# Kernel tuning notes

Hardware: AMD Instinct MI355X
Metric: run time of the kernel (lower is better)

## Reference

```python
import jax, jax.numpy as jnp
import numpy as np

N, E, D, R, H = 50000, 200000, 128, 4, 64

def setup_inputs() -> dict:
    key = jax.random.key(0)
    ks = jax.random.split(key, 12)
    s = 0.02
    return {
        'node_feature': jax.random.normal(ks[0], (N, D), dtype=jnp.float32),
        'edge_src': jax.random.randint(ks[1], (E,), 0, N, dtype=jnp.int32),
        'edge_dst': jax.random.randint(ks[2], (E,), 0, N, dtype=jnp.int32),
        'edge_type': jax.random.randint(ks[3], (E,), 0, R, dtype=jnp.int32),
        'Wr1': s * jax.random.normal(ks[4], (R, D, H), dtype=jnp.float32),
        'br1': jnp.zeros((R, H), dtype=jnp.float32),
        'Wr2': s * jax.random.normal(ks[5], (R, H, H), dtype=jnp.float32),
        'br2': jnp.zeros((R, H), dtype=jnp.float32),
        'Wr3': s * jax.random.normal(ks[6], (R, H, D), dtype=jnp.float32),
        'br3': jnp.zeros((R, D), dtype=jnp.float32),
        'Wn1': s * jax.random.normal(ks[7], ((R + 1) * D, H), dtype=jnp.float32),
        'bn1': jnp.zeros((H,), dtype=jnp.float32),
        'Wn2': s * jax.random.normal(ks[8], (H, H), dtype=jnp.float32),
        'bn2': jnp.zeros((H,), dtype=jnp.float32),
        'Wn3': s * jax.random.normal(ks[9], (H, D), dtype=jnp.float32),
        'bn3': jnp.zeros((D,), dtype=jnp.float32),
    }

def reference(node_feature, edge_src, edge_dst, edge_type,
              Wr1, br1, Wr2, br2, Wr3, br3,
              Wn1, bn1, Wn2, bn2, Wn3, bn3):
    n, d = node_feature.shape
    r = Wr1.shape[0]
    # gather source node features per edge  [E, D]
    x_src = node_feature[edge_src]
    # per-relation message MLP over all edges (masked below): relu hidden layers,
    # linear output, then outer relu as in message_function
    h = jax.nn.relu(jnp.einsum('ed,rdh->reh', x_src, Wr1) + br1[:, None, :])
    h = jax.nn.relu(jnp.einsum('reh,rhk->rek', h, Wr2) + br2[:, None, :])
    msg = jax.nn.relu(jnp.einsum('rek,rkd->red', h, Wr3) + br3[:, None, :])  # [R, E, D]
    # zero out edges not of this relation type (mirrors boolean masking)
    mask = (edge_type[None, :] == jnp.arange(r, dtype=edge_type.dtype)[:, None])
    msg = msg * mask[:, :, None].astype(msg.dtype)
    # scatter-sum messages into destination node slots  [R, N, D]
    agg = jax.vmap(lambda m: jax.ops.segment_sum(m, edge_dst, num_segments=n))(msg)
    # node_enc_input: [relu(node_feature), agg_0, ..., agg_{R-1}]  -> [N, (R+1)*D]
    node_in = jnp.concatenate(
        [jax.nn.relu(node_feature), agg.transpose(1, 0, 2).reshape(n, r * d)], axis=1)
    # node updater MLP
    h = jax.nn.relu(node_in @ Wn1 + bn1)
    h = jax.nn.relu(h @ Wn2 + bn2)
    return h @ Wn3 + bn3
```

## Files before the change

### kernel.cpp

```cpp
#include <hip/hip_runtime.h>

#define DD 128
#define HH 64
#define RR 4
#define NT 256
#define NNT 512
#define DGRID 512
#define DPART 128

typedef __attribute__((ext_vector_type(8))) __bf16 bf16x8;
typedef __attribute__((ext_vector_type(4))) __bf16 bf16x4;
typedef __attribute__((ext_vector_type(4))) float f32x4;

#define SK128 136
#define SK64  72
#define ABLK  2176

#define O_W1  0
#define O_W2  8704
#define O_W3  13312
#define O_WP  22528
#define O_ACT 31232
#define DSMEM_ELEMS 39936
#define N_W1  0
#define N_W2  8704
#define N_W3  13312
#define N_ACT 22528
#define NSMEM_ELEMS 39936

#define W1T_OFF 0
#define W2T_OFF 32768
#define W3T_OFF 49152
#define WPT_OFF 81920
#define WN1_OFF 114688
#define WN2_OFF 122880
#define WN3_OFF 126976
#define WT_TOTAL 135168

#define MFMA(a, b, c) __builtin_amdgcn_mfma_f32_16x16x32_bf16(a, b, c, 0, 0, 0)


template<int ROWS, int COLS, int STRIDE, int BLK>
__device__ __forceinline__ void stageRM(const __bf16* __restrict__ g, __bf16* s, int tid) {
    constexpr int CH = COLS / 8;
    constexpr int TOT = ROWS * CH;
    #pragma unroll
    for (int i = tid; i < TOT; i += BLK) {
        const int row = i / CH, c8 = i % CH;
        *(bf16x8*)(s + row * STRIDE + c8 * 8) = *(const bf16x8*)(g + row * COLS + c8 * 8);
    }
}

__global__ void k_prep_hist(const float* __restrict__ Wr1, const float* __restrict__ Wr2,
                            const float* __restrict__ Wr3, const float* __restrict__ Wn1,
                            const float* __restrict__ Wn2, const float* __restrict__ Wn3,
                            __bf16* __restrict__ wt,
                            const int* __restrict__ ed, int* __restrict__ dstCnt, int E) {
    int i = blockIdx.x * blockDim.x + threadIdx.x;
    if (i < E) atomicAdd(&dstCnt[ed[i]], 1);
    if (i < 32768) {
        int r = i >> 13, k = (i >> 6) & 127, n = i & 63;
        wt[W1T_OFF + r * 8192 + n * 128 + k] = (__bf16)Wr1[i];
    } else if (i < 49152) {
        int j = i - 32768; int r = j >> 12, k = (j >> 6) & 63, n = j & 63;
        wt[W2T_OFF + r * 4096 + n * 64 + k] = (__bf16)Wr2[j];
    } else if (i < 81920) {
        int j = i - 49152; int r = j >> 13, k = (j >> 7) & 63, n = j & 127;
        wt[W3T_OFF + r * 8192 + n * 64 + k] = (__bf16)Wr3[j];
    } else if (i < 122880) {
        int j = i - 81920; int row = j >> 6, n = j & 63;
        int s = row >> 7, k = row & 127;
        float v = Wn1[j];
        if (s == 0) wt[WN1_OFF + n * 128 + k] = (__bf16)v;
        else        wt[WPT_OFF + (s - 1) * 8192 + n * 128 + k] = (__bf16)v;
    } else if (i < 126976) {
        int j = i - 122880; int k = j >> 6, n = j & 63;
        wt[WN2_OFF + n * 64 + k] = (__bf16)Wn2[j];
    } else if (i < WT_TOTAL) {
        int j = i - 126976; int k = j >> 7, n = j & 127;
        wt[WN3_OFF + n * 64 + k] = (__bf16)Wn3[j];
    }
}

__global__ void k_bsum(const int* __restrict__ dstCnt, int* __restrict__ blkSum, int Nn) {
    int b = blockIdx.x, t = threadIdx.x;
    int g = b * 1024 + t * 4;
    int s = 0;
    if (g + 3 < Nn) { int4 v = *(const int4*)(dstCnt + g); s = v.x + v.y + v.z + v.w; }
    else { for (int k = 0; k < 4; k++) if (g + k < Nn) s += dstCnt[g + k]; }
    for (int off = 32; off > 0; off >>= 1) s += __shfl_down(s, off);
    __shared__ int ws[4];
    if ((t & 63) == 0) ws[t >> 6] = s;
    __syncthreads();
    if (t == 0) blkSum[b] = ws[0] + ws[1] + ws[2] + ws[3];
}

__global__ void k_mid(const int* __restrict__ blkSum, int* __restrict__ blkOff,
                      int* __restrict__ rowStart, int NB, int Nn, int E) {
    int lane = threadIdx.x;
    int s = (lane < NB) ? blkSum[lane] : 0;
    int sc = s;
    #pragma unroll
    for (int off = 1; off < 64; off <<= 1) { int u = __shfl_up(sc, off); if (lane >= off) sc += u; }
    if (lane < NB) blkOff[lane] = sc - s;
    if (lane == 0) rowStart[Nn] = E;
}

__global__ void k_wout(const int* __restrict__ dstCnt, const int* __restrict__ blkOff,
                       int* __restrict__ rowStart, int* __restrict__ dstCursor, int Nn) {
    int b = blockIdx.x, t = threadIdx.x;
    int g = b * 1024 + t * 4;
    int4 v = {0, 0, 0, 0};
    bool full = (g + 3 < Nn);
    if (full) v = *(const int4*)(dstCnt + g);
    else {
        if (g     < Nn) v.x = dstCnt[g];
        if (g + 1 < Nn) v.y = dstCnt[g + 1];
        if (g + 2 < Nn) v.z = dstCnt[g + 2];
    }
    int s = v.x + v.y + v.z + v.w;
    int lane = t & 63, wv = t >> 6;
    int sc = s;
    #pragma unroll
    for (int off = 1; off < 64; off <<= 1) { int u = __shfl_up(sc, off); if (lane >= off) sc += u; }
    __shared__ int wsum[4];
    if (lane == 63) wsum[wv] = sc;
    __syncthreads();
    int wadd = 0;
    for (int i = 0; i < wv; i++) wadd += wsum[i];
    int e0 = blkOff[b] + wadd + sc - s;
    int4 rs; rs.x = e0; rs.y = e0 + v.x; rs.z = rs.y + v.y; rs.w = rs.z + v.z;
    if (full) { *(int4*)(rowStart + g) = rs; *(int4*)(dstCursor + g) = rs; }
    else {
        int a[4] = {rs.x, rs.y, rs.z, rs.w};
        for (int k = 0; k < 4; k++) if (g + k < Nn) { rowStart[g + k] = a[k]; dstCursor[g + k] = a[k]; }
    }
}

__global__ void k_place(const int* __restrict__ et, const int* __restrict__ ed,
                        const int* __restrict__ es, int* __restrict__ dstCursor,
                        int* __restrict__ csrKey, int E, int Nn) {
    int i = blockIdx.x * blockDim.x + threadIdx.x;
    if (i < E) {
        int sl = atomicAdd(&dstCursor[ed[i]], 1);
        csrKey[sl] = et[i] * Nn + es[i];
    }
}

__global__ __launch_bounds__(NT, 2) void k_dense(
    const float* __restrict__ nf,
    const float* __restrict__ br1, const float* __restrict__ br2, const float* __restrict__ br3,
    const __bf16* __restrict__ wt, __bf16* __restrict__ ca, int Nn)
{
    extern __shared__ __bf16 smem[];
    const int r    = blockIdx.x & 3;
    const int part = blockIdx.x >> 2;
    const int tid  = threadIdx.x;
    const int w = tid >> 6;
    const int lane = tid & 63;
    const int ln = lane & 15, qd = lane >> 4;
    const int m0 = w << 4;
    __bf16* act = smem + O_ACT + w * ABLK;

    stageRM<64, 128, SK128, NT>(wt + W1T_OFF + r * 8192, smem + O_W1, tid);
    stageRM<64,  64, SK64 , NT>(wt + W2T_OFF + r * 4096, smem + O_W2, tid);
    stageRM<128, 64, SK64 , NT>(wt + W3T_OFF + r * 8192, smem + O_W3, tid);
    stageRM<64, 128, SK128, NT>(wt + WPT_OFF + r * 8192, smem + O_WP, tid);

    float bv1[4], bv2[4], bv3[8];
    #pragma unroll
    for (int nt = 0; nt < 4; nt++) {
        bv1[nt] = br1[r * HH + nt * 16 + ln];
        bv2[nt] = br2[r * HH + nt * 16 + ln];
    }
    #pragma unroll
    for (int nt = 0; nt < 8; nt++) bv3[nt] = br3[r * DD + nt * 16 + ln];

    const int T = (Nn + 63) >> 6;
    const int mx = tid >> 2, qx = tid & 3;
    __bf16* xr = act + (mx & 15) * SK128 + 32 * qx;

    float4 xv[8];
    int t = part;
    if (t < T) {
        const int node = min(t * 64 + mx, Nn - 1);
        const float4* rp = (const float4*)(nf + (size_t)node * DD) + 8 * qx;
        #pragma unroll
        for (int j = 0; j < 8; j++) xv[j] = rp[j];
    }
    __syncthreads();

    for (; t < T; t += DPART) {
        const int nb0 = t * 64;

        #pragma unroll
        for (int jj = 0; jj < 4; jj++) {
            float4 v0 = xv[2 * jj], v1 = xv[2 * jj + 1];
            bf16x8 p;
            p[0] = (__bf16)v0.x; p[1] = (__bf16)v0.y; p[2] = (__bf16)v0.z; p[3] = (__bf16)v0.w;
            p[4] = (__bf16)v1.x; p[5] = (__bf16)v1.y; p[6] = (__bf16)v1.z; p[7] = (__bf16)v1.w;
            *(bf16x8*)(xr + 8 * jj) = p;
        }
        bf16x8 ax[4];
        #pragma unroll
        for (int i = 0; i < 4; i++)
            ax[i] = *(const bf16x8*)(act + ln * SK128 + i * 32 + 8 * qd);

        const int tn = t + DPART;
        if (tn < T) {
            const int node = min(tn * 64 + mx, Nn - 1);
            const float4* rp = (const float4*)(nf + (size_t)node * DD) + 8 * qx;
            #pragma unroll
            for (int j = 0; j < 8; j++) xv[j] = rp[j];
        }

        {
            f32x4 c[4] = {};
            #pragma unroll
            for (int kk = 0; kk < 4; kk++)
                #pragma unroll
                for (int nt = 0; nt < 4; nt++) {
                    bf16x8 b = *(const bf16x8*)(smem + O_W1 + (nt * 16 + ln) * SK128 + kk * 32 + 8 * qd);
                    c[nt] = MFMA(ax[kk], b, c[nt]);
                }
            #pragma unroll
            for (int nt = 0; nt < 4; nt++)
                #pragma unroll
                for (int rg = 0; rg < 4; rg++) {
                    float v = c[nt][rg] + bv1[nt];
                    act[(qd * 4 + rg) * SK64 + nt * 16 + ln] = (__bf16)fmaxf(v, 0.f);
                }
        }
        {
            bf16x8 a0 = *(const bf16x8*)(act + ln * SK64 + 0 + 8 * qd);
            bf16x8 a1 = *(const bf16x8*)(act + ln * SK64 + 32 + 8 * qd);
            f32x4 c[4] = {};
            #pragma unroll
            for (int nt = 0; nt < 4; nt++) {
                bf16x8 b0 = *(const bf16x8*)(smem + O_W2 + (nt * 16 + ln) * SK64 + 0 + 8 * qd);
                bf16x8 b1 = *(const bf16x8*)(smem + O_W2 + (nt * 16 + ln) * SK64 + 32 + 8 * qd);
                c[nt] = MFMA(a0, b0, c[nt]);
                c[nt] = MFMA(a1, b1, c[nt]);
            }
            #pragma unroll
            for (int nt = 0; nt < 4; nt++)
                #pragma unroll
                for (int rg = 0; rg < 4; rg++) {
                    float v = c[nt][rg] + bv2[nt];
                    act[(qd * 4 + rg) * SK64 + nt * 16 + ln] = (__bf16)fmaxf(v, 0.f);
                }
        }
        {
            bf16x8 a0 = *(const bf16x8*)(act + ln * SK64 + 0 + 8 * qd);
            bf16x8 a1 = *(const bf16x8*)(act + ln * SK64 + 32 + 8 * qd);
            f32x4 c[8];
            #pragma unroll
            for (int nt = 0; nt < 8; nt++) {
                bf16x8 b0 = *(const bf16x8*)(smem + O_W3 + (nt * 16 + ln) * SK64 + 0 + 8 * qd);
                bf16x8 b1 = *(const bf16x8*)(smem + O_W3 + (nt * 16 + ln) * SK64 + 32 + 8 * qd);
                f32x4 acc = {};
                acc = MFMA(a0, b0, acc);
                acc = MFMA(a1, b1, acc);
                c[nt] = acc;
            }
            #pragma unroll
            for (int nt = 0; nt < 8; nt++)
                #pragma unroll
                for (int rg = 0; rg < 4; rg++) {
                    float v = c[nt][rg] + bv3[nt];
                    act[(qd * 4 + rg) * SK128 + nt * 16 + ln] = (__bf16)fmaxf(v, 0.f);
                }
        }
        {
            bf16x8 am[4];
            #pragma unroll
            for (int i = 0; i < 4; i++)
                am[i] = *(const bf16x8*)(act + ln * SK128 + i * 32 + 8 * qd);
            f32x4 c[4] = {};
            #pragma unroll
            for (int kk = 0; kk < 4; kk++)
                #pragma unroll
                for (int nt = 0; nt < 4; nt++) {
                    bf16x8 b = *(const bf16x8*)(smem + O_WP + (nt * 16 + ln) * SK128 + kk * 32 + 8 * qd);
                    c[nt] = MFMA(am[kk], b, c[nt]);
                }
            #pragma unroll
            for (int rg = 0; rg < 4; rg++) {
                const int node = nb0 + m0 + qd * 4 + rg;
                if (node < Nn) {
                    bf16x4 v;
                    v[0] = (__bf16)c[0][rg]; v[1] = (__bf16)c[1][rg];
                    v[2] = (__bf16)c[2][rg]; v[3] = (__bf16)c[3][rg];
                    *(bf16x4*)(ca + ((size_t)r * Nn + node) * HH + ln * 4) = v;
                }
            }
        }
    }
}

__global__ __launch_bounds__(NNT, 4) void k_node(
    const float* __restrict__ nf,
    const float* __restrict__ bn1, const float* __restrict__ bn2, const float* __restrict__ bn3,
    const __bf16* __restrict__ wt, const __bf16* __restrict__ ca,
    const int* __restrict__ rowStart, const int* __restrict__ csrKey,
    float* __restrict__ out, int Nn)
{
    extern __shared__ __bf16 smem[];
    const int nb0 = blockIdx.x * 128;
    const int tid = threadIdx.x;
    const int w = tid >> 6;
    const int lane = tid & 63;
    const int ln = lane & 15, qd = lane >> 4;
    const int m0 = w << 4;
    __bf16* act = smem + N_ACT + w * ABLK;

    stageRM<64, 128, SK128, NNT>(wt + WN1_OFF, smem + N_W1, tid);
    stageRM<64,  64, SK64 , NNT>(wt + WN2_OFF, smem + N_W2, tid);
    stageRM<128, 64, SK64 , NNT>(wt + WN3_OFF, smem + N_W3, tid);
    {
        const int m = tid >> 2, q = tid & 3;
        const int node = min(nb0 + m, Nn - 1);
        const float4* rp = (const float4*)(nf + (size_t)node * DD) + 8 * q;
        __bf16* xr = act + (m & 15) * SK128 + 32 * q;
        #pragma unroll
        for (int jj = 0; jj < 4; jj++) {
            float4 v0 = rp[2 * jj], v1 = rp[2 * jj + 1];
            bf16x8 p;
            p[0] = (__bf16)fmaxf(v0.x, 0.f); p[1] = (__bf16)fmaxf(v0.y, 0.f);
            p[2] = (__bf16)fmaxf(v0.z, 0.f); p[3] = (__bf16)fmaxf(v0.w, 0.f);
            p[4] = (__bf16)fmaxf(v1.x, 0.f); p[5] = (__bf16)fmaxf(v1.y, 0.f);
            p[6] = (__bf16)fmaxf(v1.z, 0.f); p[7] = (__bf16)fmaxf(v1.w, 0.f);
            *(bf16x8*)(xr + 8 * jj) = p;
        }
    }
    bf16x8 ax[4];
    #pragma unroll
    for (int i = 0; i < 4; i++)
        ax[i] = *(const bf16x8*)(act + ln * SK128 + i * 32 + 8 * qd);

    float bv1[4], bv2[4], bv3[8];
    #pragma unroll
    for (int nt = 0; nt < 4; nt++) { bv1[nt] = bn1[nt * 16 + ln]; bv2[nt] = bn2[nt * 16 + ln]; }
    #pragma unroll
    for (int nt = 0; nt < 8; nt++) bv3[nt] = bn3[nt * 16 + ln];

    float agg[4][4] = {};
    {
        const int base = nb0 + m0 + qd * 4;
        int rs[5];
        #pragma unroll
        for (int j = 0; j < 5; j++) rs[j] = rowStart[min(base + j, Nn)];
        int cur[4];
        #pragma unroll
        for (int rg = 0; rg < 4; rg++) cur[rg] = rs[rg];
        const __bf16* cab = ca + ln * 4;

        while (true) {
            int k0[4], k1[4];
            bool v0[4], v1[4];
            bool any = false;
            #pragma unroll
            for (int rg = 0; rg < 4; rg++) {
                const int c0 = cur[rg], e1 = rs[rg + 1];
                v0[rg] = c0 < e1;
                v1[rg] = c0 + 1 < e1;
                if (v0[rg]) k0[rg] = csrKey[c0];
                if (v1[rg]) k1[rg] = csrKey[c0 + 1];
                cur[rg] = c0 + (v0[rg] ? 1 : 0) + (v1[rg] ? 1 : 0);
                any |= v0[rg];
            }
            if (!any) break;
            #pragma unroll
            for (int rg = 0; rg < 4; rg++) {
                if (v0[rg]) {
                    const bf16x4 x = *(const bf16x4*)(cab + (size_t)k0[rg] * HH);
                    agg[rg][0] += (float)x[0]; agg[rg][1] += (float)x[1];
                    agg[rg][2] += (float)x[2]; agg[rg][3] += (float)x[3];
                }
                if (v1[rg]) {
                    const bf16x4 x = *(const bf16x4*)(cab + (size_t)k1[rg] * HH);
                    agg[rg][0] += (float)x[0]; agg[rg][1] += (float)x[1];
                    agg[rg][2] += (float)x[2]; agg[rg][3] += (float)x[3];
                }
            }
        }
    }
    __syncthreads();

    {
        f32x4 c[4] = {};
        #pragma unroll
        for (int kk = 0; kk < 4; kk++)
            #pragma unroll
            for (int nt = 0; nt < 4; nt++) {
                bf16x8 b = *(const bf16x8*)(smem + N_W1 + (nt * 16 + ln) * SK128 + kk * 32 + 8 * qd);
                c[nt] = MFMA(ax[kk], b, c[nt]);
            }
        #pragma unroll
        for (int nt = 0; nt < 4; nt++)
            #pragma unroll
            for (int rg = 0; rg < 4; rg++) {
                float v = c[nt][rg] + bv1[nt] + agg[rg][nt];
                act[(qd * 4 + rg) * SK64 + nt * 16 + ln] = (__bf16)fmaxf(v, 0.f);
            }
    }
    {
        bf16x8 a0 = *(const bf16x8*)(act + ln * SK64 + 0 + 8 * qd);
        bf16x8 a1 = *(const bf16x8*)(act + ln * SK64 + 32 + 8 * qd);
        f32x4 c[4] = {};
        #pragma unroll
        for (int nt = 0; nt < 4; nt++) {
            bf16x8 b0 = *(const bf16x8*)(smem + N_W2 + (nt * 16 + ln) * SK64 + 0 + 8 * qd);
            bf16x8 b1 = *(const bf16x8*)(smem + N_W2 + (nt * 16 + ln) * SK64 + 32 + 8 * qd);
            c[nt] = MFMA(a0, b0, c[nt]);
            c[nt] = MFMA(a1, b1, c[nt]);
        }
        #pragma unroll
        for (int nt = 0; nt < 4; nt++)
            #pragma unroll
            for (int rg = 0; rg < 4; rg++) {
                float v = c[nt][rg] + bv2[nt];
                act[(qd * 4 + rg) * SK64 + nt * 16 + ln] = (__bf16)fmaxf(v, 0.f);
            }
    }
    {
        bf16x8 a0 = *(const bf16x8*)(act + ln * SK64 + 0 + 8 * qd);
        bf16x8 a1 = *(const bf16x8*)(act + ln * SK64 + 32 + 8 * qd);
        f32x4 c[8];
        #pragma unroll
        for (int nt = 0; nt < 8; nt++) {
            bf16x8 b0 = *(const bf16x8*)(smem + N_W3 + (nt * 16 + ln) * SK64 + 0 + 8 * qd);
            bf16x8 b1 = *(const bf16x8*)(smem + N_W3 + (nt * 16 + ln) * SK64 + 32 + 8 * qd);
            f32x4 acc = {};
            acc = MFMA(a0, b0, acc);
            acc = MFMA(a1, b1, acc);
            c[nt] = acc;
        }
        #pragma unroll
        for (int rg = 0; rg < 4; rg++) {
            const int node = nb0 + m0 + qd * 4 + rg;
            if (node < Nn) {
                float* op = out + (size_t)node * DD;
                #pragma unroll
                for (int nt = 0; nt < 8; nt++)
                    op[nt * 16 + ln] = c[nt][rg] + bv3[nt];
            }
        }
    }
}

extern "C" void kernel_launch(void* const* d_in, const int* in_sizes, int n_in,
                              void* d_out, int out_size, void* d_ws, size_t ws_size,
                              hipStream_t stream) {
    const float* nf  = (const float*)d_in[0];
    const int*   es  = (const int*)d_in[1];
    const int*   ed  = (const int*)d_in[2];
    const int*   et  = (const int*)d_in[3];
    const float* Wr1 = (const float*)d_in[4];
    const float* br1 = (const float*)d_in[5];
    const float* Wr2 = (const float*)d_in[6];
    const float* br2 = (const float*)d_in[7];
    const float* Wr3 = (const float*)d_in[8];
    const float* br3 = (const float*)d_in[9];
    const float* Wn1 = (const float*)d_in[10];
    const float* bn1 = (const float*)d_in[11];
    const float* Wn2 = (const float*)d_in[12];
    const float* bn2 = (const float*)d_in[13];
    const float* Wn3 = (const float*)d_in[14];
    const float* bn3 = (const float*)d_in[15];
    float* out = (float*)d_out;

    const int Nn = in_sizes[0] / DD;
    const int E  = in_sizes[1];
    const int NB = (Nn + 1023) / 1024;

    int* p = (int*)d_ws;
    int* dstCnt    = p;                 p += Nn;
    int* dstCursor = p;                 p += Nn;
    int* rowStart  = p;                 p += Nn + 1;
    int* blkSum    = p;                 p += 64;
    int* blkOff    = p;                 p += 64;
    int* csrKey    = p;                 p += E;
    p += ((8 - ((p - (int*)d_ws) & 7)) & 7);
    __bf16* wbf = (__bf16*)p;           p += (WT_TOTAL + 1) / 2;
    __bf16* ca  = (__bf16*)p;

    hipFuncSetAttribute((const void*)k_dense,
                        hipFuncAttributeMaxDynamicSharedMemorySize,
                        DSMEM_ELEMS * (int)sizeof(__bf16));
    hipFuncSetAttribute((const void*)k_node,
                        hipFuncAttributeMaxDynamicSharedMemorySize,
                        NSMEM_ELEMS * (int)sizeof(__bf16));

    hipMemsetAsync((void*)dstCnt, 0, (size_t)Nn * sizeof(int), stream);

    const int nb = (E + NT - 1) / NT;
    k_prep_hist<<<nb, NT, 0, stream>>>(Wr1, Wr2, Wr3, Wn1, Wn2, Wn3, wbf, ed, dstCnt, E);
    k_bsum <<<NB, 256, 0, stream>>>(dstCnt, blkSum, Nn);
    k_mid  <<<1, 64, 0, stream>>>(blkSum, blkOff, rowStart, NB, Nn, E);
    k_wout <<<NB, 256, 0, stream>>>(dstCnt, blkOff, rowStart, dstCursor, Nn);
    k_place<<<nb, NT, 0, stream>>>(et, ed, es, dstCursor, csrKey, E, Nn);

    k_dense<<<DGRID, NT, DSMEM_ELEMS * sizeof(__bf16), stream>>>(nf, br1, br2, br3, wbf, ca, Nn);
    k_node <<<(Nn + 127) / 128, NNT, NSMEM_ELEMS * sizeof(__bf16), stream>>>(
        nf, bn1, bn2, bn3, wbf, ca, rowStart, csrKey, out, Nn);
}
```

Before: 183.4 us.

## Fuse all stages into one persistent kernel with grid-wide barriers

Replaces the seven-kernel pipeline (weight prep, histogram, scans, placement, dense per-relation MLP, node MLP) with one persistent kernel of 512 blocks that separates phases with an atomic-counter grid barrier. It also overlaps the destination histogram with the dense message MLP inside the same phase. The aim is to remove launch overhead and inter-kernel gaps. In exchange it depends on all 512 blocks being co-resident, otherwise the barrier deadlocks. The node phase now runs on 256-thread blocks instead of the previous 512-thread launch.

```diff
diff --git a/kernel.cpp b/kernel.cpp
--- a/kernel.cpp
+++ b/kernel.cpp
@@ -4,7 +4,6 @@
 #define HH 64
 #define RR 4
 #define NT 256
-#define NNT 512
 #define DGRID 512
 #define DPART 128
 
@@ -26,7 +25,6 @@
 #define N_W2  8704
 #define N_W3  13312
 #define N_ACT 22528
-#define NSMEM_ELEMS 39936
 
 #define W1T_OFF 0
 #define W2T_OFF 32768
@@ -40,6 +38,18 @@
 #define MFMA(a, b, c) __builtin_amdgcn_mfma_f32_16x16x32_bf16(a, b, c, 0, 0, 0)
 
 
+__device__ __forceinline__ void gbar(int* bar, int target) {
+    __syncthreads();
+    if (threadIdx.x == 0) {
+        __threadfence();
+        __hip_atomic_fetch_add(bar, 1, __ATOMIC_ACQ_REL, __HIP_MEMORY_SCOPE_AGENT);
+        while (__hip_atomic_load(bar, __ATOMIC_ACQUIRE, __HIP_MEMORY_SCOPE_AGENT) < target)
+            __builtin_amdgcn_s_sleep(2);
+        __threadfence();
+    }
+    __syncthreads();
+}
+
 template<int ROWS, int COLS, int STRIDE, int BLK>
 __device__ __forceinline__ void stageRM(const __bf16* __restrict__ g, __bf16* s, int tid) {
     constexpr int CH = COLS / 8;
@@ -51,399 +61,400 @@
     }
 }
 
-__global__ void k_prep_hist(const float* __restrict__ Wr1, const float* __restrict__ Wr2,
-                            const float* __restrict__ Wr3, const float* __restrict__ Wn1,
-                            const float* __restrict__ Wn2, const float* __restrict__ Wn3,
-                            __bf16* __restrict__ wt,
-                            const int* __restrict__ ed, int* __restrict__ dstCnt, int E) {
-    int i = blockIdx.x * blockDim.x + threadIdx.x;
-    if (i < E) atomicAdd(&dstCnt[ed[i]], 1);
-    if (i < 32768) {
-        int r = i >> 13, k = (i >> 6) & 127, n = i & 63;
-        wt[W1T_OFF + r * 8192 + n * 128 + k] = (__bf16)Wr1[i];
-    } else if (i < 49152) {
-        int j = i - 32768; int r = j >> 12, k = (j >> 6) & 63, n = j & 63;
-        wt[W2T_OFF + r * 4096 + n * 64 + k] = (__bf16)Wr2[j];
-    } else if (i < 81920) {
-        int j = i - 49152; int r = j >> 13, k = (j >> 7) & 63, n = j & 127;
-        wt[W3T_OFF + r * 8192 + n * 64 + k] = (__bf16)Wr3[j];
-    } else if (i < 122880) {
-        int j = i - 81920; int row = j >> 6, n = j & 63;
-        int s = row >> 7, k = row & 127;
-        float v = Wn1[j];
-        if (s == 0) wt[WN1_OFF + n * 128 + k] = (__bf16)v;
-        else        wt[WPT_OFF + (s - 1) * 8192 + n * 128 + k] = (__bf16)v;
-    } else if (i < 126976) {
-        int j = i - 122880; int k = j >> 6, n = j & 63;
-        wt[WN2_OFF + n * 64 + k] = (__bf16)Wn2[j];
-    } else if (i < WT_TOTAL) {
-        int j = i - 126976; int k = j >> 7, n = j & 127;
-        wt[WN3_OFF + n * 64 + k] = (__bf16)Wn3[j];
-    }
-}
-
-__global__ void k_bsum(const int* __restrict__ dstCnt, int* __restrict__ blkSum, int Nn) {
-    int b = blockIdx.x, t = threadIdx.x;
-    int g = b * 1024 + t * 4;
-    int s = 0;
-    if (g + 3 < Nn) { int4 v = *(const int4*)(dstCnt + g); s = v.x + v.y + v.z + v.w; }
-    else { for (int k = 0; k < 4; k++) if (g + k < Nn) s += dstCnt[g + k]; }
-    for (int off = 32; off > 0; off >>= 1) s += __shfl_down(s, off);
-    __shared__ int ws[4];
-    if ((t & 63) == 0) ws[t >> 6] = s;
-    __syncthreads();
-    if (t == 0) blkSum[b] = ws[0] + ws[1] + ws[2] + ws[3];
-}
-
-__global__ void k_mid(const int* __restrict__ blkSum, int* __restrict__ blkOff,
-                      int* __restrict__ rowStart, int NB, int Nn, int E) {
-    int lane = threadIdx.x;
-    int s = (lane < NB) ? blkSum[lane] : 0;
-    int sc = s;
-    #pragma unroll
-    for (int off = 1; off < 64; off <<= 1) { int u = __shfl_up(sc, off); if (lane >= off) sc += u; }
-    if (lane < NB) blkOff[lane] = sc - s;
-    if (lane == 0) rowStart[Nn] = E;
-}
-
-__global__ void k_wout(const int* __restrict__ dstCnt, const int* __restrict__ blkOff,
-                       int* __restrict__ rowStart, int* __restrict__ dstCursor, int Nn) {
-    int b = blockIdx.x, t = threadIdx.x;
-    int g = b * 1024 + t * 4;
-    int4 v = {0, 0, 0, 0};
-    bool full = (g + 3 < Nn);
-    if (full) v = *(const int4*)(dstCnt + g);
-    else {
-        if (g     < Nn) v.x = dstCnt[g];
-        if (g + 1 < Nn) v.y = dstCnt[g + 1];
-        if (g + 2 < Nn) v.z = dstCnt[g + 2];
-    }
-    int s = v.x + v.y + v.z + v.w;
-    int lane = t & 63, wv = t >> 6;
-    int sc = s;
-    #pragma unroll
-    for (int off = 1; off < 64; off <<= 1) { int u = __shfl_up(sc, off); if (lane >= off) sc += u; }
-    __shared__ int wsum[4];
-    if (lane == 63) wsum[wv] = sc;
-    __syncthreads();
-    int wadd = 0;
-    for (int i = 0; i < wv; i++) wadd += wsum[i];
-    int e0 = blkOff[b] + wadd + sc - s;
-    int4 rs; rs.x = e0; rs.y = e0 + v.x; rs.z = rs.y + v.y; rs.w = rs.z + v.z;
-    if (full) { *(int4*)(rowStart + g) = rs; *(int4*)(dstCursor + g) = rs; }
-    else {
-        int a[4] = {rs.x, rs.y, rs.z, rs.w};
-        for (int k = 0; k < 4; k++) if (g + k < Nn) { rowStart[g + k] = a[k]; dstCursor[g + k] = a[k]; }
-    }
-}
-
-__global__ void k_place(const int* __restrict__ et, const int* __restrict__ ed,
-                        const int* __restrict__ es, int* __restrict__ dstCursor,
-                        int* __restrict__ csrKey, int E, int Nn) {
-    int i = blockIdx.x * blockDim.x + threadIdx.x;
-    if (i < E) {
-        int sl = atomicAdd(&dstCursor[ed[i]], 1);
-        csrKey[sl] = et[i] * Nn + es[i];
-    }
-}
-
-__global__ __launch_bounds__(NT, 2) void k_dense(
+__global__ __launch_bounds__(NT, 2) void k_mega(
     const float* __restrict__ nf,
-    const float* __restrict__ br1, const float* __restrict__ br2, const float* __restrict__ br3,
-    const __bf16* __restrict__ wt, __bf16* __restrict__ ca, int Nn)
+    const int* __restrict__ es, const int* __restrict__ ed, const int* __restrict__ et,
+    const float* __restrict__ Wr1, const float* __restrict__ br1,
+    const float* __restrict__ Wr2, const float* __restrict__ br2,
+    const float* __restrict__ Wr3, const float* __restrict__ br3,
+    const float* __restrict__ Wn1, const float* __restrict__ bn1,
+    const float* __restrict__ Wn2, const float* __restrict__ bn2,
+    const float* __restrict__ Wn3, const float* __restrict__ bn3,
+    __bf16* __restrict__ wt, __bf16* __restrict__ ca,
+    int* bar, int* __restrict__ dstCnt, int* __restrict__ dstCursor,
+    int* __restrict__ rowStart, int* __restrict__ blkSum,
+    int* __restrict__ csrKey, float* __restrict__ out,
+    int Nn, int E, int NB)
 {
     extern __shared__ __bf16 smem[];
-    const int r    = blockIdx.x & 3;
-    const int part = blockIdx.x >> 2;
+
     const int tid  = threadIdx.x;
+    const int gtid = blockIdx.x * NT + tid;
+    const int GSZ  = DGRID * NT;
     const int w = tid >> 6;
     const int lane = tid & 63;
     const int ln = lane & 15, qd = lane >> 4;
     const int m0 = w << 4;
-    __bf16* act = smem + O_ACT + w * ABLK;
-
-    stageRM<64, 128, SK128, NT>(wt + W1T_OFF + r * 8192, smem + O_W1, tid);
-    stageRM<64,  64, SK64 , NT>(wt + W2T_OFF + r * 4096, smem + O_W2, tid);
-    stageRM<128, 64, SK64 , NT>(wt + W3T_OFF + r * 8192, smem + O_W3, tid);
-    stageRM<64, 128, SK128, NT>(wt + WPT_OFF + r * 8192, smem + O_WP, tid);
-
-    float bv1[4], bv2[4], bv3[8];
-    #pragma unroll
-    for (int nt = 0; nt < 4; nt++) {
-        bv1[nt] = br1[r * HH + nt * 16 + ln];
-        bv2[nt] = br2[r * HH + nt * 16 + ln];
-    }
-    #pragma unroll
-    for (int nt = 0; nt < 8; nt++) bv3[nt] = br3[r * DD + nt * 16 + ln];
-
-    const int T = (Nn + 63) >> 6;
-    const int mx = tid >> 2, qx = tid & 3;
-    __bf16* xr = act + (mx & 15) * SK128 + 32 * qx;
-
-    float4 xv[8];
-    int t = part;
-    if (t < T) {
-        const int node = min(t * 64 + mx, Nn - 1);
-        const float4* rp = (const float4*)(nf + (size_t)node * DD) + 8 * qx;
+
+    for (int i = gtid; i < WT_TOTAL; i += GSZ) {
+        if (i < 32768) {
+            int r = i >> 13, k = (i >> 6) & 127, n = i & 63;
+            wt[W1T_OFF + r * 8192 + n * 128 + k] = (__bf16)Wr1[i];
+        } else if (i < 49152) {
+            int j = i - 32768; int r = j >> 12, k = (j >> 6) & 63, n = j & 63;
+            wt[W2T_OFF + r * 4096 + n * 64 + k] = (__bf16)Wr2[j];
+        } else if (i < 81920) {
+            int j = i - 49152; int r = j >> 13, k = (j >> 7) & 63, n = j & 127;
+            wt[W3T_OFF + r * 8192 + n * 64 + k] = (__bf16)Wr3[j];
+        } else if (i < 122880) {
+            int j = i - 81920; int row = j >> 6, n = j & 63;
+            int s = row >> 7, k = row & 127;
+            float v = Wn1[j];
+            if (s == 0) wt[WN1_OFF + n * 128 + k] = (__bf16)v;
+            else        wt[WPT_OFF + (s - 1) * 8192 + n * 128 + k] = (__bf16)v;
+        } else if (i < 126976) {
+            int j = i - 122880; int k = j >> 6, n = j & 63;
+            wt[WN2_OFF + n * 64 + k] = (__bf16)Wn2[j];
+        } else {
+            int j = i - 126976; int k = j >> 7, n = j & 127;
+            wt[WN3_OFF + n * 64 + k] = (__bf16)Wn3[j];
+        }
+    }
+    gbar(bar, DGRID * 1);
+
+    for (int i = gtid; i < E; i += GSZ) atomicAdd(&dstCnt[ed[i]], 1);
+    {
+        const int r    = blockIdx.x & 3;
+        const int part = blockIdx.x >> 2;
+        __bf16* act = smem + O_ACT + w * ABLK;
+
+        stageRM<64, 128, SK128, NT>(wt + W1T_OFF + r * 8192, smem + O_W1, tid);
+        stageRM<64,  64, SK64 , NT>(wt + W2T_OFF + r * 4096, smem + O_W2, tid);
+        stageRM<128, 64, SK64 , NT>(wt + W3T_OFF + r * 8192, smem + O_W3, tid);
+        stageRM<64, 128, SK128, NT>(wt + WPT_OFF + r * 8192, smem + O_WP, tid);
+
+        float bv1[4], bv2[4], bv3[8];
         #pragma unroll
-        for (int j = 0; j < 8; j++) xv[j] = rp[j];
-    }
-    __syncthreads();
-
-    for (; t < T; t += DPART) {
-        const int nb0 = t * 64;
-
+        for (int nt = 0; nt < 4; nt++) {
+            bv1[nt] = br1[r * HH + nt * 16 + ln];
+            bv2[nt] = br2[r * HH + nt * 16 + ln];
+        }
         #pragma unroll
-        for (int jj = 0; jj < 4; jj++) {
-            float4 v0 = xv[2 * jj], v1 = xv[2 * jj + 1];
-            bf16x8 p;
-            p[0] = (__bf16)v0.x; p[1] = (__bf16)v0.y; p[2] = (__bf16)v0.z; p[3] = (__bf16)v0.w;
-            p[4] = (__bf16)v1.x; p[5] = (__bf16)v1.y; p[6] = (__bf16)v1.z; p[7] = (__bf16)v1.w;
-            *(bf16x8*)(xr + 8 * jj) = p;
-        }
-        bf16x8 ax[4];
-        #pragma unroll
-        for (int i = 0; i < 4; i++)
-            ax[i] = *(const bf16x8*)(act + ln * SK128 + i * 32 + 8 * qd);
-
-        const int tn = t + DPART;
-        if (tn < T) {
-            const int node = min(tn * 64 + mx, Nn - 1);
+        for (int nt = 0; nt < 8; nt++) bv3[nt] = br3[r * DD + nt * 16 + ln];
+
+        const int T = (Nn + 63) >> 6;
+        const int mx = tid >> 2, qx = tid & 3;
+        __bf16* xr = act + (mx & 15) * SK128 + 32 * qx;
+
+        float4 xv[8];
+        int t = part;
+        if (t < T) {
+            const int node = min(t * 64 + mx, Nn - 1);
             const float4* rp = (const float4*)(nf + (size_t)node * DD) + 8 * qx;
             #pragma unroll
             for (int j = 0; j < 8; j++) xv[j] = rp[j];
         }
-
-        {
-            f32x4 c[4] = {};
+        __syncthreads();
+
+        for (; t < T; t += DPART) {
+            const int nb0 = t * 64;
             #pragma unroll
-            for (int kk = 0; kk < 4; kk++)
-                #pragma unroll
-                for (int nt = 0; nt < 4; nt++) {
-                    bf16x8 b = *(const bf16x8*)(smem + O_W1 + (nt * 16 + ln) * SK128 + kk * 32 + 8 * qd);
-                    c[nt] = MFMA(ax[kk], b, c[nt]);
-                }
-            #pragma unroll
-            for (int nt = 0; nt < 4; nt++)
-                #pragma unroll
-                for (int rg = 0; rg < 4; rg++) {
-                    float v = c[nt][rg] + bv1[nt];
-                    act[(qd * 4 + rg) * SK64 + nt * 16 + ln] = (__bf16)fmaxf(v, 0.f);
-                }
-        }
-        {
-            bf16x8 a0 = *(const bf16x8*)(act + ln * SK64 + 0 + 8 * qd);
-            bf16x8 a1 = *(const bf16x8*)(act + ln * SK64 + 32 + 8 * qd);
-            f32x4 c[4] = {};
-            #pragma unroll
-            for (int nt = 0; nt < 4; nt++) {
-                bf16x8 b0 = *(const bf16x8*)(smem + O_W2 + (nt * 16 + ln) * SK64 + 0 + 8 * qd);
-                bf16x8 b1 = *(const bf16x8*)(smem + O_W2 + (nt * 16 + ln) * SK64 + 32 + 8 * qd);
-                c[nt] = MFMA(a0, b0, c[nt]);
-                c[nt] = MFMA(a1, b1, c[nt]);
-            }
-            #pragma unroll
-            for (int nt = 0; nt < 4; nt++)
-                #pragma unroll
-                for (int rg = 0; rg < 4; rg++) {
-                    float v = c[nt][rg] + bv2[nt];
-                    act[(qd * 4 + rg) * SK64 + nt * 16 + ln] = (__bf16)fmaxf(v, 0.f);
-                }
-        }
-        {
-            bf16x8 a0 = *(const bf16x8*)(act + ln * SK64 + 0 + 8 * qd);
-            bf16x8 a1 = *(const bf16x8*)(act + ln * SK64 + 32 + 8 * qd);
-            f32x4 c[8];
-            #pragma unroll
-            for (int nt = 0; nt < 8; nt++) {
-                bf16x8 b0 = *(const bf16x8*)(smem + O_W3 + (nt * 16 + ln) * SK64 + 0 + 8 * qd);
-                bf16x8 b1 = *(const bf16x8*)(smem + O_W3 + (nt * 16 + ln) * SK64 + 32 + 8 * qd);
-                f32x4 acc = {};
-                acc = MFMA(a0, b0, acc);
-                acc = MFMA(a1, b1, acc);
-                c[nt] = acc;
-            }
-            #pragma unroll
-            for (int nt = 0; nt < 8; nt++)
-                #pragma unroll
-                for (int rg = 0; rg < 4; rg++) {
-                    float v = c[nt][rg] + bv3[nt];
-                    act[(qd * 4 + rg) * SK128 + nt * 16 + ln] = (__bf16)fmaxf(v, 0.f);
-                }
-        }
-        {
-            bf16x8 am[4];
+            for (int jj = 0; jj < 4; jj++) {
+                float4 v0 = xv[2 * jj], v1 = xv[2 * jj + 1];
+                bf16x8 p;
+                p[0] = (__bf16)v0.x; p[1] = (__bf16)v0.y; p[2] = (__bf16)v0.z; p[3] = (__bf16)v0.w;
+                p[4] = (__bf16)v1.x; p[5] = (__bf16)v1.y; p[6] = (__bf16)v1.z; p[7] = (__bf16)v1.w;
+                *(bf16x8*)(xr + 8 * jj) = p;
+            }
+            bf16x8 ax[4];
             #pragma unroll
             for (int i = 0; i < 4; i++)
-                am[i] = *(const bf16x8*)(act + ln * SK128 + i * 32 + 8 * qd);
-            f32x4 c[4] = {};
+                ax[i] = *(const bf16x8*)(act + ln * SK128 + i * 32 + 8 * qd);
+
+            const int tn = t + DPART;
+            if (tn < T) {
+                const int node = min(tn * 64 + mx, Nn - 1);
+                const float4* rp = (const float4*)(nf + (size_t)node * DD) + 8 * qx;
+                #pragma unroll
+                for (int j = 0; j < 8; j++) xv[j] = rp[j];
+            }
+
+            {
+                f32x4 c[4] = {};
+                #pragma unroll
+                for (int kk = 0; kk < 4; kk++)
+                    #pragma unroll
+                    for (int nt = 0; nt < 4; nt++) {
+                        bf16x8 b = *(const bf16x8*)(smem + O_W1 + (nt * 16 + ln) * SK128 + kk * 32 + 8 * qd);
+                        c[nt] = MFMA(ax[kk], b, c[nt]);
+                    }
+                #pragma unroll
+                for (int nt = 0; nt < 4; nt++)
+                    #pragma unroll
+                    for (int rg = 0; rg < 4; rg++) {
+                        float v = c[nt][rg] + bv1[nt];
+                        act[(qd * 4 + rg) * SK64 + nt * 16 + ln] = (__bf16)fmaxf(v, 0.f);
+                    }
+            }
+            {
+                bf16x8 a0 = *(const bf16x8*)(act + ln * SK64 + 0 + 8 * qd);
+                bf16x8 a1 = *(const bf16x8*)(act + ln * SK64 + 32 + 8 * qd);
+                f32x4 c[4] = {};
+                #pragma unroll
+                for (int nt = 0; nt < 4; nt++) {
+                    bf16x8 b0 = *(const bf16x8*)(smem + O_W2 + (nt * 16 + ln) * SK64 + 0 + 8 * qd);
+                    bf16x8 b1 = *(const bf16x8*)(smem + O_W2 + (nt * 16 + ln) * SK64 + 32 + 8 * qd);
+                    c[nt] = MFMA(a0, b0, c[nt]);
+                    c[nt] = MFMA(a1, b1, c[nt]);
+                }
+                #pragma unroll
+                for (int nt = 0; nt < 4; nt++)
+                    #pragma unroll
+                    for (int rg = 0; rg < 4; rg++) {
+                        float v = c[nt][rg] + bv2[nt];
+                        act[(qd * 4 + rg) * SK64 + nt * 16 + ln] = (__bf16)fmaxf(v, 0.f);
+                    }
+            }
+            {
+                bf16x8 a0 = *(const bf16x8*)(act + ln * SK64 + 0 + 8 * qd);
+                bf16x8 a1 = *(const bf16x8*)(act + ln * SK64 + 32 + 8 * qd);
+                f32x4 c[8];
+                #pragma unroll
+                for (int nt = 0; nt < 8; nt++) {
+                    bf16x8 b0 = *(const bf16x8*)(smem + O_W3 + (nt * 16 + ln) * SK64 + 0 + 8 * qd);
+                    bf16x8 b1 = *(const bf16x8*)(smem + O_W3 + (nt * 16 + ln) * SK64 + 32 + 8 * qd);
+                    f32x4 acc = {};
+                    acc = MFMA(a0, b0, acc);
+                    acc = MFMA(a1, b1, acc);
+                    c[nt] = acc;
+                }
+                #pragma unroll
+                for (int nt = 0; nt < 8; nt++)
+                    #pragma unroll
+                    for (int rg = 0; rg < 4; rg++) {
+                        float v = c[nt][rg] + bv3[nt];
+                        act[(qd * 4 + rg) * SK128 + nt * 16 + ln] = (__bf16)fmaxf(v, 0.f);
+                    }
+            }
+            {
+                bf16x8 am[4];
+                #pragma unroll
+                for (int i = 0; i < 4; i++)
+                    am[i] = *(const bf16x8*)(act + ln * SK128 + i * 32 + 8 * qd);
+                f32x4 c[4] = {};
+                #pragma unroll
+                for (int kk = 0; kk < 4; kk++)
+                    #pragma unroll
+                    for (int nt = 0; nt < 4; nt++) {
+                        bf16x8 b = *(const bf16x8*)(smem + O_WP + (nt * 16 + ln) * SK128 + kk * 32 + 8 * qd);
+                        c[nt] = MFMA(am[kk], b, c[nt]);
+                    }
+                #pragma unroll
+                for (int rg = 0; rg < 4; rg++) {
+                    const int node = nb0 + m0 + qd * 4 + rg;
+                    if (node < Nn) {
+                        bf16x4 v;
+                        v[0] = (__bf16)c[0][rg]; v[1] = (__bf16)c[1][rg];
+                        v[2] = (__bf16)c[2][rg]; v[3] = (__bf16)c[3][rg];
+                        *(bf16x4*)(ca + ((size_t)r * Nn + node) * HH + ln * 4) = v;
+                    }
+                }
+            }
+        }
+    }
+    gbar(bar, DGRID * 2);
+
+    if (blockIdx.x < NB) {
+        int* iw = (int*)smem;
+        const int g = blockIdx.x * 1024 + tid * 4;
+        int s = 0;
+        if (g + 3 < Nn) { int4 v = *(const int4*)(dstCnt + g); s = v.x + v.y + v.z + v.w; }
+        else { for (int k = 0; k < 4; k++) if (g + k < Nn) s += dstCnt[g + k]; }
+        for (int off = 32; off > 0; off >>= 1) s += __shfl_down(s, off);
+        __syncthreads();
+        if ((tid & 63) == 0) iw[tid >> 6] = s;
+        __syncthreads();
+        if (tid == 0) blkSum[blockIdx.x] = iw[0] + iw[1] + iw[2] + iw[3];
+    }
+    gbar(bar, DGRID * 3);
+
+    if (blockIdx.x < NB) {
+        int* iw = (int*)smem;
+        if (tid < 64) {
+            int s = (tid < NB) ? blkSum[tid] : 0;
+            int sc = s;
             #pragma unroll
-            for (int kk = 0; kk < 4; kk++)
+            for (int off = 1; off < 64; off <<= 1) { int u = __shfl_up(sc, off); if (tid >= off) sc += u; }
+            int ex = (blockIdx.x == 0) ? 0 : __shfl(sc, blockIdx.x - 1);
+            if (tid == 0) iw[4] = ex;
+        }
+        __syncthreads();
+        const int e0base = iw[4];
+
+        const int g = blockIdx.x * 1024 + tid * 4;
+        int4 v = {0, 0, 0, 0};
+        bool full = (g + 3 < Nn);
+        if (full) v = *(const int4*)(dstCnt + g);
+        else {
+            if (g     < Nn) v.x = dstCnt[g];
+            if (g + 1 < Nn) v.y = dstCnt[g + 1];
+            if (g + 2 < Nn) v.z = dstCnt[g + 2];
+        }
+        int s = v.x + v.y + v.z + v.w;
+        int lane2 = tid & 63, wv = tid >> 6;
+        int sc = s;
+        #pragma unroll
+        for (int off = 1; off < 64; off <<= 1) { int u = __shfl_up(sc, off); if (lane2 >= off) sc += u; }
+        if (lane2 == 63) iw[wv] = sc;
+        __syncthreads();
+        int wadd = 0;
+        for (int i = 0; i < wv; i++) wadd += iw[i];
+        int e0 = e0base + wadd + sc - s;
+        int4 rs; rs.x = e0; rs.y = e0 + v.x; rs.z = rs.y + v.y; rs.w = rs.z + v.z;
+        if (full) { *(int4*)(rowStart + g) = rs; *(int4*)(dstCursor + g) = rs; }
+        else {
+            int a[4] = {rs.x, rs.y, rs.z, rs.w};
+            for (int k = 0; k < 4; k++) if (g + k < Nn) { rowStart[g + k] = a[k]; dstCursor[g + k] = a[k]; }
+        }
+    }
+    if (gtid == 0) rowStart[Nn] = E;
+    gbar(bar, DGRID * 4);
+
+    for (int i = gtid; i < E; i += GSZ) {
+        int sl = atomicAdd(&dstCursor[ed[i]], 1);
+        csrKey[sl] = et[i] * Nn + es[i];
+    }
+    gbar(bar, DGRID * 5);
+
+    {
+        __bf16* act = smem + N_ACT + w * ABLK;
+        stageRM<64, 128, SK128, NT>(wt + WN1_OFF, smem + N_W1, tid);
+        stageRM<64,  64, SK64 , NT>(wt + WN2_OFF, smem + N_W2, tid);
+        stageRM<128, 64, SK64 , NT>(wt + WN3_OFF, smem + N_W3, tid);
+
+        float bv1[4], bv2[4], bv3[8];
+        #pragma unroll
+        for (int nt = 0; nt < 4; nt++) { bv1[nt] = bn1[nt * 16 + ln]; bv2[nt] = bn2[nt * 16 + ln]; }
+        #pragma unroll
+        for (int nt = 0; nt < 8; nt++) bv3[nt] = bn3[nt * 16 + ln];
+
+        const int T = (Nn + 63) >> 6;
+        const int mx = tid >> 2, qx = tid & 3;
+        __bf16* xr = act + (mx & 15) * SK128 + 32 * qx;
+        __syncthreads();
+
+        for (int t = blockIdx.x; t < T; t += DGRID) {
+            const int nb0 = t * 64;
+            {
+                const int node = min(nb0 + mx, Nn - 1);
+                const float4* rp = (const float4*)(nf + (size_t)node * DD) + 8 * qx;
+                #pragma unroll
+                for (int jj = 0; jj < 4; jj++) {
+                    float4 v0 = rp[2 * jj], v1 = rp[2 * jj + 1];
+                    bf16x8 p;
+                    p[0] = (__bf16)fmaxf(v0.x, 0.f); p[1] = (__bf16)fmaxf(v0.y, 0.f);
+                    p[2] = (__bf16)fmaxf(v0.z, 0.f); p[3] = (__bf16)fmaxf(v0.w, 0.f);
+                    p[4] = (__bf16)fmaxf(v1.x, 0.f); p[5] = (__bf16)fmaxf(v1.y, 0.f);
+                    p[6] = (__bf16)fmaxf(v1.z, 0.f); p[7] = (__bf16)fmaxf(v1.w, 0.f);
+                    *(bf16x8*)(xr + 8 * jj) = p;
+                }
+            }
+            bf16x8 ax[4];
+            #pragma unroll
+            for (int i = 0; i < 4; i++)
+                ax[i] = *(const bf16x8*)(act + ln * SK128 + i * 32 + 8 * qd);
+
+            float agg[4][4] = {};
+            {
+                const int base = nb0 + m0 + qd * 4;
+                int rs[5];
+                #pragma unroll
+                for (int j = 0; j < 5; j++) rs[j] = rowStart[min(base + j, Nn)];
+                int cur[4];
+                #pragma unroll
+                for (int rg = 0; rg < 4; rg++) cur[rg] = rs[rg];
+                const __bf16* cab = ca + ln * 4;
+
+                while (true) {
+                    int k0[4], k1[4];
+                    bool v0[4], v1[4];
+                    bool any = false;
+                    #pragma unroll
+                    for (int rg = 0; rg < 4; rg++) {
+                        const int c0 = cur[rg], e1 = rs[rg + 1];
+                        v0[rg] = c0 < e1;
+                        v1[rg] = c0 + 1 < e1;
+                        if (v0[rg]) k0[rg] = csrKey[c0];
+                        if (v1[rg]) k1[rg] = csrKey[c0 + 1];
+                        cur[rg] = c0 + (v0[rg] ? 1 : 0) + (v1[rg] ? 1 : 0);
+                        any |= v0[rg];
+                    }
+                    if (!any) break;
+                    #pragma unroll
+                    for (int rg = 0; rg < 4; rg++) {
+                        if (v0[rg]) {
+                            const bf16x4 x = *(const bf16x4*)(cab + (size_t)k0[rg] * HH);
+                            agg[rg][0] += (float)x[0]; agg[rg][1] += (float)x[1];
+                            agg[rg][2] += (float)x[2]; agg[rg][3] += (float)x[3];
+                        }
+                        if (v1[rg]) {
+                            const bf16x4 x = *(const bf16x4*)(cab + (size_t)k1[rg] * HH);
+                            agg[rg][0] += (float)x[0]; agg[rg][1] += (float)x[1];
+                            agg[rg][2] += (float)x[2]; agg[rg][3] += (float)x[3];
+                        }
+                    }
+                }
+            }
+
+            {
+                f32x4 c[4] = {};
+                #pragma unroll
+                for (int kk = 0; kk < 4; kk++)
+                    #pragma unroll
+                    for (int nt = 0; nt < 4; nt++) {
+                        bf16x8 b = *(const bf16x8*)(smem + N_W1 + (nt * 16 + ln) * SK128 + kk * 32 + 8 * qd);
+                        c[nt] = MFMA(ax[kk], b, c[nt]);
+                    }
+                #pragma unroll
+                for (int nt = 0; nt < 4; nt++)
+                    #pragma unroll
+                    for (int rg = 0; rg < 4; rg++) {
+                        float v = c[nt][rg] + bv1[nt] + agg[rg][nt];
+                        act[(qd * 4 + rg) * SK64 + nt * 16 + ln] = (__bf16)fmaxf(v, 0.f);
+                    }
+            }
+            {
+                bf16x8 a0 = *(const bf16x8*)(act + ln * SK64 + 0 + 8 * qd);
+                bf16x8 a1 = *(const bf16x8*)(act + ln * SK64 + 32 + 8 * qd);
+                f32x4 c[4] = {};
                 #pragma unroll
                 for (int nt = 0; nt < 4; nt++) {
-                    bf16x8 b = *(const bf16x8*)(smem + O_WP + (nt * 16 + ln) * SK128 + kk * 32 + 8 * qd);
-                    c[nt] = MFMA(am[kk], b, c[nt]);
-                }
-            #pragma unroll
-            for (int rg = 0; rg < 4; rg++) {
-                const int node = nb0 + m0 + qd * 4 + rg;
-                if (node < Nn) {
-                    bf16x4 v;
-                    v[0] = (__bf16)c[0][rg]; v[1] = (__bf16)c[1][rg];
-                    v[2] = (__bf16)c[2][rg]; v[3] = (__bf16)c[3][rg];
-                    *(bf16x4*)(ca + ((size_t)r * Nn + node) * HH + ln * 4) = v;
-                }
-            }
-        }
-    }
-}
-
-__global__ __launch_bounds__(NNT, 4) void k_node(
-    const float* __restrict__ nf,
-    const float* __restrict__ bn1, const float* __restrict__ bn2, const float* __restrict__ bn3,
-    const __bf16* __restrict__ wt, const __bf16* __restrict__ ca,
-    const int* __restrict__ rowStart, const int* __restrict__ csrKey,
-    float* __restrict__ out, int Nn)
-{
-    extern __shared__ __bf16 smem[];
-    const int nb0 = blockIdx.x * 128;
-    const int tid = threadIdx.x;
-    const int w = tid >> 6;
-    const int lane = tid & 63;
-    const int ln = lane & 15, qd = lane >> 4;
-    const int m0 = w << 4;
-    __bf16* act = smem + N_ACT + w * ABLK;
-
-    stageRM<64, 128, SK128, NNT>(wt + WN1_OFF, smem + N_W1, tid);
-    stageRM<64,  64, SK64 , NNT>(wt + WN2_OFF, smem + N_W2, tid);
-    stageRM<128, 64, SK64 , NNT>(wt + WN3_OFF, smem + N_W3, tid);
-    {
-        const int m = tid >> 2, q = tid & 3;
-        const int node = min(nb0 + m, Nn - 1);
-        const float4* rp = (const float4*)(nf + (size_t)node * DD) + 8 * q;
-        __bf16* xr = act + (m & 15) * SK128 + 32 * q;
-        #pragma unroll
-        for (int jj = 0; jj < 4; jj++) {
-            float4 v0 = rp[2 * jj], v1 = rp[2 * jj + 1];
-            bf16x8 p;
-            p[0] = (__bf16)fmaxf(v0.x, 0.f); p[1] = (__bf16)fmaxf(v0.y, 0.f);
-            p[2] = (__bf16)fmaxf(v0.z, 0.f); p[3] = (__bf16)fmaxf(v0.w, 0.f);
-            p[4] = (__bf16)fmaxf(v1.x, 0.f); p[5] = (__bf16)fmaxf(v1.y, 0.f);
-            p[6] = (__bf16)fmaxf(v1.z, 0.f); p[7] = (__bf16)fmaxf(v1.w, 0.f);
-            *(bf16x8*)(xr + 8 * jj) = p;
-        }
-    }
-    bf16x8 ax[4];
-    #pragma unroll
-    for (int i = 0; i < 4; i++)
-        ax[i] = *(const bf16x8*)(act + ln * SK128 + i * 32 + 8 * qd);
-
-    float bv1[4], bv2[4], bv3[8];
-    #pragma unroll
-    for (int nt = 0; nt < 4; nt++) { bv1[nt] = bn1[nt * 16 + ln]; bv2[nt] = bn2[nt * 16 + ln]; }
-    #pragma unroll
-    for (int nt = 0; nt < 8; nt++) bv3[nt] = bn3[nt * 16 + ln];
-
-    float agg[4][4] = {};
-    {
-        const int base = nb0 + m0 + qd * 4;
-        int rs[5];
-        #pragma unroll
-        for (int j = 0; j < 5; j++) rs[j] = rowStart[min(base + j, Nn)];
-        int cur[4];
-        #pragma unroll
-        for (int rg = 0; rg < 4; rg++) cur[rg] = rs[rg];
-        const __bf16* cab = ca + ln * 4;
-
-        while (true) {
-            int k0[4], k1[4];
-            bool v0[4], v1[4];
-            bool any = false;
-            #pragma unroll
-            for (int rg = 0; rg < 4; rg++) {
-                const int c0 = cur[rg], e1 = rs[rg + 1];
-                v0[rg] = c0 < e1;
-                v1[rg] = c0 + 1 < e1;
-                if (v0[rg]) k0[rg] = csrKey[c0];
-                if (v1[rg]) k1[rg] = csrKey[c0 + 1];
-                cur[rg] = c0 + (v0[rg] ? 1 : 0) + (v1[rg] ? 1 : 0);
-                any |= v0[rg];
-            }
-            if (!any) break;
-            #pragma unroll
-            for (int rg = 0; rg < 4; rg++) {
-                if (v0[rg]) {
-                    const bf16x4 x = *(const bf16x4*)(cab + (size_t)k0[rg] * HH);
-                    agg[rg][0] += (float)x[0]; agg[rg][1] += (float)x[1];
-                    agg[rg][2] += (float)x[2]; agg[rg][3] += (float)x[3];
-                }
-                if (v1[rg]) {
-                    const bf16x4 x = *(const bf16x4*)(cab + (size_t)k1[rg] * HH);
-                    agg[rg][0] += (float)x[0]; agg[rg][1] += (float)x[1];
-                    agg[rg][2] += (float)x[2]; agg[rg][3] += (float)x[3];
-                }
-            }
-        }
-    }
-    __syncthreads();
-
-    {
-        f32x4 c[4] = {};
-        #pragma unroll
-        for (int kk = 0; kk < 4; kk++)
-            #pragma unroll
-            for (int nt = 0; nt < 4; nt++) {
-                bf16x8 b = *(const bf16x8*)(smem + N_W1 + (nt * 16 + ln) * SK128 + kk * 32 + 8 * qd);
-                c[nt] = MFMA(ax[kk], b, c[nt]);
-            }
-        #pragma unroll
-        for (int nt = 0; nt < 4; nt++)
-            #pragma unroll
-            for (int rg = 0; rg < 4; rg++) {
-                float v = c[nt][rg] + bv1[nt] + agg[rg][nt];
-                act[(qd * 4 + rg) * SK64 + nt * 16 + ln] = (__bf16)fmaxf(v, 0.f);
-            }
-    }
-    {
-        bf16x8 a0 = *(const bf16x8*)(act + ln * SK64 + 0 + 8 * qd);
-        bf16x8 a1 = *(const bf16x8*)(act + ln * SK64 + 32 + 8 * qd);
-        f32x4 c[4] = {};
-        #pragma unroll
-        for (int nt = 0; nt < 4; nt++) {
-            bf16x8 b0 = *(const bf16x8*)(smem + N_W2 + (nt * 16 + ln) * SK64 + 0 + 8 * qd);
-            bf16x8 b1 = *(const bf16x8*)(smem + N_W2 + (nt * 16 + ln) * SK64 + 32 + 8 * qd);
-            c[nt] = MFMA(a0, b0, c[nt]);
-            c[nt] = MFMA(a1, b1, c[nt]);
-        }
-        #pragma unroll
-        for (int nt = 0; nt < 4; nt++)
-            #pragma unroll
-            for (int rg = 0; rg < 4; rg++) {
-                float v = c[nt][rg] + bv2[nt];
-                act[(qd * 4 + rg) * SK64 + nt * 16 + ln] = (__bf16)fmaxf(v, 0.f);
-            }
-    }
-    {
-        bf16x8 a0 = *(const bf16x8*)(act + ln * SK64 + 0 + 8 * qd);
-        bf16x8 a1 = *(const bf16x8*)(act + ln * SK64 + 32 + 8 * qd);
-        f32x4 c[8];
-        #pragma unroll
-        for (int nt = 0; nt < 8; nt++) {
-            bf16x8 b0 = *(const bf16x8*)(smem + N_W3 + (nt * 16 + ln) * SK64 + 0 + 8 * qd);
-            bf16x8 b1 = *(const bf16x8*)(smem + N_W3 + (nt * 16 + ln) * SK64 + 32 + 8 * qd);
-            f32x4 acc = {};
-            acc = MFMA(a0, b0, acc);
-            acc = MFMA(a1, b1, acc);
-            c[nt] = acc;
-        }
-        #pragma unroll
-        for (int rg = 0; rg < 4; rg++) {
-            const int node = nb0 + m0 + qd * 4 + rg;
-            if (node < Nn) {
-                float* op = out + (size_t)node * DD;
-                #pragma unroll
-                for (int nt = 0; nt < 8; nt++)
-                    op[nt * 16 + ln] = c[nt][rg] + bv3[nt];
+                    bf16x8 b0 = *(const bf16x8*)(smem + N_W2 + (nt * 16 + ln) * SK64 + 0 + 8 * qd);
+                    bf16x8 b1 = *(const bf16x8*)(smem + N_W2 + (nt * 16 + ln) * SK64 + 32 + 8 * qd);
+                    c[nt] = MFMA(a0, b0, c[nt]);
+                    c[nt] = MFMA(a1, b1, c[nt]);
+                }
+                #pragma unroll
+                for (int nt = 0; nt < 4; nt++)
+                    #pragma unroll
+                    for (int rg = 0; rg < 4; rg++) {
+                        float v = c[nt][rg] + bv2[nt];
+                        act[(qd * 4 + rg) * SK64 + nt * 16 + ln] = (__bf16)fmaxf(v, 0.f);
+                    }
+            }
+            {
+                bf16x8 a0 = *(const bf16x8*)(act + ln * SK64 + 0 + 8 * qd);
+                bf16x8 a1 = *(const bf16x8*)(act + ln * SK64 + 32 + 8 * qd);
+                f32x4 c[8];
+                #pragma unroll
+                for (int nt = 0; nt < 8; nt++) {
+                    bf16x8 b0 = *(const bf16x8*)(smem + N_W3 + (nt * 16 + ln) * SK64 + 0 + 8 * qd);
+                    bf16x8 b1 = *(const bf16x8*)(smem + N_W3 + (nt * 16 + ln) * SK64 + 32 + 8 * qd);
+                    f32x4 acc = {};
+                    acc = MFMA(a0, b0, acc);
+                    acc = MFMA(a1, b1, acc);
+                    c[nt] = acc;
+                }
+                #pragma unroll
+                for (int rg = 0; rg < 4; rg++) {
+                    const int node = nb0 + m0 + qd * 4 + rg;
+                    if (node < Nn) {
+                        float* op = out + (size_t)node * DD;
+                        #pragma unroll
+                        for (int nt = 0; nt < 8; nt++)
+                            op[nt * 16 + ln] = c[nt][rg] + bv3[nt];
+                    }
+                }
             }
         }
     }
@@ -470,38 +481,30 @@
     const float* bn3 = (const float*)d_in[15];
     float* out = (float*)d_out;
 
-    const int Nn = in_sizes[0] / DD;
-    const int E  = in_sizes[1];
-    const int NB = (Nn + 1023) / 1024;
+    int Nn = in_sizes[0] / DD;
+    int E  = in_sizes[1];
+    int NB = (Nn + 1023) / 1024;
 
     int* p = (int*)d_ws;
+    int* bar       = p;                 p += 4;
     int* dstCnt    = p;                 p += Nn;
     int* dstCursor = p;                 p += Nn;
     int* rowStart  = p;                 p += Nn + 1;
     int* blkSum    = p;                 p += 64;
-    int* blkOff    = p;                 p += 64;
     int* csrKey    = p;                 p += E;
     p += ((8 - ((p - (int*)d_ws) & 7)) & 7);
     __bf16* wbf = (__bf16*)p;           p += (WT_TOTAL + 1) / 2;
     __bf16* ca  = (__bf16*)p;
 
-    hipFuncSetAttribute((const void*)k_dense,
+    hipFuncSetAttribute((const void*)k_mega,
                         hipFuncAttributeMaxDynamicSharedMemorySize,
                         DSMEM_ELEMS * (int)sizeof(__bf16));
-    hipFuncSetAttribute((const void*)k_node,
-                        hipFuncAttributeMaxDynamicSharedMemorySize,
-                        NSMEM_ELEMS * (int)sizeof(__bf16));
-
-    hipMemsetAsync((void*)dstCnt, 0, (size_t)Nn * sizeof(int), stream);
-
-    const int nb = (E + NT - 1) / NT;
-    k_prep_hist<<<nb, NT, 0, stream>>>(Wr1, Wr2, Wr3, Wn1, Wn2, Wn3, wbf, ed, dstCnt, E);
-    k_bsum <<<NB, 256, 0, stream>>>(dstCnt, blkSum, Nn);
-    k_mid  <<<1, 64, 0, stream>>>(blkSum, blkOff, rowStart, NB, Nn, E);
-    k_wout <<<NB, 256, 0, stream>>>(dstCnt, blkOff, rowStart, dstCursor, Nn);
-    k_place<<<nb, NT, 0, stream>>>(et, ed, es, dstCursor, csrKey, E, Nn);
-
-    k_dense<<<DGRID, NT, DSMEM_ELEMS * sizeof(__bf16), stream>>>(nf, br1, br2, br3, wbf, ca, Nn);
-    k_node <<<(Nn + 127) / 128, NNT, NSMEM_ELEMS * sizeof(__bf16), stream>>>(
-        nf, bn1, bn2, bn3, wbf, ca, rowStart, csrKey, out, Nn);
+
+    hipMemsetAsync(d_ws, 0, (size_t)(4 + Nn) * sizeof(int), stream);
+
+    k_mega<<<DGRID, NT, DSMEM_ELEMS * sizeof(__bf16), stream>>>(
+        nf, es, ed, et, Wr1, br1, Wr2, br2, Wr3, br3,
+        Wn1, bn1, Wn2, bn2, Wn3, bn3,
+        wbf, ca, bar, dstCnt, dstCursor, rowStart, blkSum, csrKey, out,
+        Nn, E, NB);
 }
```

Result: slower. 431.0 us (+135.1%).
